# Kernel tuning notes

Measured on AMD Instinct MI355X. Metric: run time of the kernel, lower is better.

## Reference

```python
import jax, jax.numpy as jnp
import numpy as np


def setup_inputs() -> dict:
    key = jax.random.key(0)
    k1, k2, k3, k4, k5 = jax.random.split(key, 5)
    B, T_en, T_de, D, U = 8, 256, 256, 256, 256
    return {
        "en_seq": jax.random.normal(k1, (B, T_en, D), dtype=jnp.float32),
        "de_seq": jax.random.normal(k2, (B, T_de, D), dtype=jnp.float32),
        "w_en": jax.random.normal(k3, (D, U), dtype=jnp.float32) * (1.0 / np.sqrt(D)),
        "w_de": jax.random.normal(k4, (D, U), dtype=jnp.float32) * (1.0 / np.sqrt(D)),
        "nu": jax.random.normal(k5, (U, 1), dtype=jnp.float32) * (1.0 / np.sqrt(U)),
    }


def reference(en_seq, de_seq, w_en, w_de, nu):
    # Additive (Bahdanau) cross attention, faithful to the Keras layer.
    # The Keras code materializes a (B, T_de*T_en, units) tensor via
    # repeat/repeat_elements with layout index = de*T_en + en; broadcasting
    # att_en over the de axis and att_de over the en axis reproduces it.
    att_en = jnp.einsum('bed,du->beu', en_seq, w_en)       # (B, T_en, U)
    att_de = jnp.einsum('btd,du->btu', de_seq, w_de)       # (B, T_de, U)
    co_m = att_en[:, None, :, :] + att_de[:, :, None, :]   # (B, T_de, T_en, U)
    mu = jnp.einsum('bteu,uo->bteo', jnp.tanh(co_m), nu)[..., 0]  # (B, T_de, T_en)
    alphas = jax.nn.softmax(mu, axis=-1)                   # softmax over encoder steps
    sum_en = jnp.einsum('bte,bed->btd', alphas, en_seq)    # (B, T_de, D)
    return de_seq + sum_en
```

## Files before the change

kernel.cpp:

```cpp
#include <hip/hip_runtime.h>


#define C2LOG2E 2.8853900817779268f

__device__ __forceinline__ const float* uptr(const float* p) {
    unsigned long long v = (unsigned long long)p;
    unsigned lo = __builtin_amdgcn_readfirstlane((unsigned)v);
    unsigned hi = __builtin_amdgcn_readfirstlane((unsigned)(v >> 32));
    return (const float*)((((unsigned long long)hi) << 32) | lo);
}

__global__ __launch_bounds__(256, 2) void gemm2(
    const float* __restrict__ en, const float* __restrict__ de,
    const float* __restrict__ w_en, const float* __restrict__ w_de,
    float* __restrict__ att_enT, float* __restrict__ att_de)
{
    __shared__ float xs[8 * 256];

    const int isDe = blockIdx.x >> 8;
    const int rb   = blockIdx.x & 255;
    const float* x = isDe ? de : en;
    const float* w = isDe ? w_de : w_en;

    const int tid  = threadIdx.x;
    const int lane = tid & 63;
    const int wv   = __builtin_amdgcn_readfirstlane(tid >> 6);
    const int r0   = rb * 8 + wv * 2;
    const int c0   = lane << 2;

    const float* ar0 = uptr(x + r0 * 256);
    const float* ar1 = uptr(x + r0 * 256 + 256);

    float4 acc0{0,0,0,0}, acc1{0,0,0,0};

    float4 wb[4], wn[4];
    #pragma unroll
    for (int j = 0; j < 4; ++j)
        wb[j] = *(const float4*)(w + j * 256 + c0);

    for (int k0 = 0; k0 < 256; k0 += 4) {
        if (k0 < 252) {
            #pragma unroll
            for (int j = 0; j < 4; ++j)
                wn[j] = *(const float4*)(w + (k0 + 4 + j) * 256 + c0);
        }
        #pragma unroll
        for (int j = 0; j < 4; ++j) {
            const int k = k0 + j;
            const float a0 = ar0[k];
            const float a1 = ar1[k];
            acc0.x = fmaf(a0, wb[j].x, acc0.x);
            acc0.y = fmaf(a0, wb[j].y, acc0.y);
            acc0.z = fmaf(a0, wb[j].z, acc0.z);
            acc0.w = fmaf(a0, wb[j].w, acc0.w);
            acc1.x = fmaf(a1, wb[j].x, acc1.x);
            acc1.y = fmaf(a1, wb[j].y, acc1.y);
            acc1.z = fmaf(a1, wb[j].z, acc1.z);
            acc1.w = fmaf(a1, wb[j].w, acc1.w);
        }
        #pragma unroll
        for (int j = 0; j < 4; ++j) wb[j] = wn[j];
    }

    const float s = C2LOG2E;
    acc0.x *= s; acc0.y *= s; acc0.z *= s; acc0.w *= s;
    acc1.x *= s; acc1.y *= s; acc1.z *= s; acc1.w *= s;

    if (isDe) {
        float* y = att_de + r0 * 256 + c0;
        *(float4*)(y)       = acc0;
        *(float4*)(y + 256) = acc1;
    } else {
        *(float4*)&xs[(wv * 2 + 0) * 256 + c0] = acc0;
        *(float4*)&xs[(wv * 2 + 1) * 256 + c0] = acc1;
        __syncthreads();
        const int b  = rb >> 5;
        const int er = (rb & 31) * 8;
        const int u  = tid;
        float4 lo, hi;
        lo.x = xs[0 * 256 + u]; lo.y = xs[1 * 256 + u];
        lo.z = xs[2 * 256 + u]; lo.w = xs[3 * 256 + u];
        hi.x = xs[4 * 256 + u]; hi.y = xs[5 * 256 + u];
        hi.z = xs[6 * 256 + u]; hi.w = xs[7 * 256 + u];
        float* yT = att_enT + b * 65536 + u * 256 + er;
        *(float4*)(yT)     = lo;
        *(float4*)(yT + 4) = hi;
    }
}

__global__ __launch_bounds__(256, 4) void attn_kernel(
    const float* __restrict__ att_enT,
    const float* __restrict__ att_de,
    const float* __restrict__ en_seq,
    const float* __restrict__ de_seq,
    const float* __restrict__ nu,
    float* __restrict__ out)
{
    const int blk  = blockIdx.x;
    const int b    = blk & 7;
    const int t0   = (blk >> 3) << 1;
    const int tid  = threadIdx.x;
    const int lane = tid & 63;
    const int wv   = __builtin_amdgcn_readfirstlane(tid >> 6);

    __shared__ float s_mu[2][256];
    __shared__ float s_al[2][256];

    const float* aw  = att_enT + b * 65536 + (wv << 6) + lane;
    const float* ad0 = uptr(att_de + (b * 256 + t0) * 256);
    const float* ad1 = uptr(att_de + (b * 256 + t0) * 256 + 256);
    const float* nuu = uptr(nu);

    float acc0 = 0.f, acc1 = 0.f;
    float av[8], avn[8];
    #pragma unroll
    for (int j = 0; j < 8; ++j) av[j] = aw[j << 8];

    for (int u0 = 0; u0 < 256; u0 += 8) {
        if (u0 < 248) {
            #pragma unroll
            for (int j = 0; j < 8; ++j) avn[j] = aw[(u0 + 8 + j) << 8];
        }
        #pragma unroll
        for (int g = 0; g < 2; ++g) {
            const int ub = u0 + g * 4;
            const float n0 = nuu[ub + 0], n1 = nuu[ub + 1];
            const float n2 = nuu[ub + 2], n3 = nuu[ub + 3];
            const float nS01 = n0 + n1, nS23 = n2 + n3;
            const float a0 = av[g * 4 + 0], a1 = av[g * 4 + 1];
            const float a2 = av[g * 4 + 2], a3 = av[g * 4 + 3];
            {
                const float E0 = __builtin_amdgcn_exp2f(a0 + ad0[ub + 0]);
                const float E1 = __builtin_amdgcn_exp2f(a1 + ad0[ub + 1]);
                const float E2 = __builtin_amdgcn_exp2f(a2 + ad0[ub + 2]);
                const float E3 = __builtin_amdgcn_exp2f(a3 + ad0[ub + 3]);
                const float A0 = E0 + 1.f, A1 = E1 + 1.f;
                const float A2 = E2 + 1.f, A3 = E3 + 1.f;
                const float p01 = A0 * A1, p23 = A2 * A3;
                const float n01 = fmaf(n0, E1, fmaf(n1, E0, nS01));
                const float n23 = fmaf(n2, E3, fmaf(n3, E2, nS23));
                const float num = fmaf(n23, p01, n01 * p23);
                acc0 = fmaf(num, __builtin_amdgcn_rcpf(p01 * p23), acc0);
            }
            {
                const float E0 = __builtin_amdgcn_exp2f(a0 + ad1[ub + 0]);
                const float E1 = __builtin_amdgcn_exp2f(a1 + ad1[ub + 1]);
                const float E2 = __builtin_amdgcn_exp2f(a2 + ad1[ub + 2]);
                const float E3 = __builtin_amdgcn_exp2f(a3 + ad1[ub + 3]);
                const float A0 = E0 + 1.f, A1 = E1 + 1.f;
                const float A2 = E2 + 1.f, A3 = E3 + 1.f;
                const float p01 = A0 * A1, p23 = A2 * A3;
                const float n01 = fmaf(n0, E1, fmaf(n1, E0, nS01));
                const float n23 = fmaf(n2, E3, fmaf(n3, E2, nS23));
                const float num = fmaf(n23, p01, n01 * p23);
                acc1 = fmaf(num, __builtin_amdgcn_rcpf(p01 * p23), acc1);
            }
        }
        #pragma unroll
        for (int j = 0; j < 8; ++j) av[j] = avn[j];
    }
    const int eidx = (wv << 6) + lane;
    s_mu[0][eidx] = acc0;
    s_mu[1][eidx] = acc1;
    __syncthreads();

    if (wv < 2) {
        const float4 a = *(const float4*)&s_mu[wv][lane << 2];
        float mn = fminf(fminf(a.x, a.y), fminf(a.z, a.w));
        #pragma unroll
        for (int off = 32; off > 0; off >>= 1)
            mn = fminf(mn, __shfl_xor(mn, off, 64));
        const float p0 = __builtin_amdgcn_exp2f((mn - a.x) * C2LOG2E);
        const float p1 = __builtin_amdgcn_exp2f((mn - a.y) * C2LOG2E);
        const float p2 = __builtin_amdgcn_exp2f((mn - a.z) * C2LOG2E);
        const float p3 = __builtin_amdgcn_exp2f((mn - a.w) * C2LOG2E);
        float ssum = (p0 + p1) + (p2 + p3);
        #pragma unroll
        for (int off = 32; off > 0; off >>= 1)
            ssum += __shfl_xor(ssum, off, 64);
        const float inv = __builtin_amdgcn_rcpf(ssum);
        float4 al; al.x = p0 * inv; al.y = p1 * inv;
        al.z = p2 * inv; al.w = p3 * inv;
        *(float4*)&s_al[wv][lane << 2] = al;
    }
    __syncthreads();

    const float* en_b = en_seq + b * 65536 + tid;
    float o0 = 0.f, o1 = 0.f;
    for (int e0 = 0; e0 < 256; e0 += 8) {
        float v[8];
        #pragma unroll
        for (int j = 0; j < 8; ++j) v[j] = en_b[(e0 + j) << 8];
        #pragma unroll
        for (int q = 0; q < 2; ++q) {
            const int eb = e0 + q * 4;
            const float4 A0 = *(const float4*)&s_al[0][eb];
            const float4 A1 = *(const float4*)&s_al[1][eb];
            o0 = fmaf(A0.x, v[q*4+0], o0); o1 = fmaf(A1.x, v[q*4+0], o1);
            o0 = fmaf(A0.y, v[q*4+1], o0); o1 = fmaf(A1.y, v[q*4+1], o1);
            o0 = fmaf(A0.z, v[q*4+2], o0); o1 = fmaf(A1.z, v[q*4+2], o1);
            o0 = fmaf(A0.w, v[q*4+3], o0); o1 = fmaf(A1.w, v[q*4+3], o1);
        }
    }
    const int base = (b * 256 + t0) * 256 + tid;
    out[base]       = de_seq[base]       + o0;
    out[base + 256] = de_seq[base + 256] + o1;
}

extern "C" void kernel_launch(void* const* d_in, const int* in_sizes, int n_in,
                              void* d_out, int out_size, void* d_ws, size_t ws_size,
                              hipStream_t stream) {
    const float* en_seq = (const float*)d_in[0];
    const float* de_seq = (const float*)d_in[1];
    const float* w_en   = (const float*)d_in[2];
    const float* w_de   = (const float*)d_in[3];
    const float* nu     = (const float*)d_in[4];
    float* out = (float*)d_out;

    float* att_enT = (float*)d_ws;
    float* att_de  = att_enT + 8 * 256 * 256;

    gemm2<<<512, 256, 0, stream>>>(en_seq, de_seq, w_en, w_de, att_enT, att_de);
    attn_kernel<<<1024, 256, 0, stream>>>(att_enT, att_de, en_seq, de_seq,
                                          nu, out);
}
```

Measured before the change: 123.2 us.

## Precompute exponentials of projections and factor exp(a+b) into products

```diff
diff --git a/kernel.cpp b/kernel.cpp
--- a/kernel.cpp
+++ b/kernel.cpp
@@ -10,87 +10,100 @@
     return (const float*)((((unsigned long long)hi) << 32) | lo);
 }
 
-__global__ __launch_bounds__(256, 2) void gemm2(
+__global__ __launch_bounds__(256, 4) void gemm2(
     const float* __restrict__ en, const float* __restrict__ de,
     const float* __restrict__ w_en, const float* __restrict__ w_de,
-    float* __restrict__ att_enT, float* __restrict__ att_de)
+    float* __restrict__ att_enT4, float* __restrict__ att_de_exp)
 {
-    __shared__ float xs[8 * 256];
-
-    const int isDe = blockIdx.x >> 8;
-    const int rb   = blockIdx.x & 255;
+    __shared__ float part[4 * 4 * 256];
+
+    const int isDe = blockIdx.x >> 9;
+    const int rb   = blockIdx.x & 511;
     const float* x = isDe ? de : en;
     const float* w = isDe ? w_de : w_en;
 
     const int tid  = threadIdx.x;
     const int lane = tid & 63;
     const int wv   = __builtin_amdgcn_readfirstlane(tid >> 6);
-    const int r0   = rb * 8 + wv * 2;
+    const int r0   = rb * 4;
     const int c0   = lane << 2;
-
-    const float* ar0 = uptr(x + r0 * 256);
-    const float* ar1 = uptr(x + r0 * 256 + 256);
-
-    float4 acc0{0,0,0,0}, acc1{0,0,0,0};
+    const int k0   = wv << 6;
+
+    const float* ar0 = uptr(x + (r0 + 0) * 256 + k0);
+    const float* ar1 = uptr(x + (r0 + 1) * 256 + k0);
+    const float* ar2 = uptr(x + (r0 + 2) * 256 + k0);
+    const float* ar3 = uptr(x + (r0 + 3) * 256 + k0);
+    const float* wk  = w + k0 * 256 + c0;
+
+    float4 acc0{0,0,0,0}, acc1{0,0,0,0}, acc2{0,0,0,0}, acc3{0,0,0,0};
 
     float4 wb[4], wn[4];
     #pragma unroll
     for (int j = 0; j < 4; ++j)
-        wb[j] = *(const float4*)(w + j * 256 + c0);
-
-    for (int k0 = 0; k0 < 256; k0 += 4) {
-        if (k0 < 252) {
+        wb[j] = *(const float4*)(wk + j * 256);
+
+    for (int kk = 0; kk < 64; kk += 4) {
+        if (kk < 60) {
             #pragma unroll
             for (int j = 0; j < 4; ++j)
-                wn[j] = *(const float4*)(w + (k0 + 4 + j) * 256 + c0);
+                wn[j] = *(const float4*)(wk + (kk + 4 + j) * 256);
         }
         #pragma unroll
         for (int j = 0; j < 4; ++j) {
-            const int k = k0 + j;
-            const float a0 = ar0[k];
-            const float a1 = ar1[k];
-            acc0.x = fmaf(a0, wb[j].x, acc0.x);
-            acc0.y = fmaf(a0, wb[j].y, acc0.y);
-            acc0.z = fmaf(a0, wb[j].z, acc0.z);
-            acc0.w = fmaf(a0, wb[j].w, acc0.w);
-            acc1.x = fmaf(a1, wb[j].x, acc1.x);
-            acc1.y = fmaf(a1, wb[j].y, acc1.y);
-            acc1.z = fmaf(a1, wb[j].z, acc1.z);
-            acc1.w = fmaf(a1, wb[j].w, acc1.w);
+            const int k = kk + j;
+            const float a0 = ar0[k], a1 = ar1[k];
+            const float a2 = ar2[k], a3 = ar3[k];
+            acc0.x = fmaf(a0, wb[j].x, acc0.x); acc0.y = fmaf(a0, wb[j].y, acc0.y);
+            acc0.z = fmaf(a0, wb[j].z, acc0.z); acc0.w = fmaf(a0, wb[j].w, acc0.w);
+            acc1.x = fmaf(a1, wb[j].x, acc1.x); acc1.y = fmaf(a1, wb[j].y, acc1.y);
+            acc1.z = fmaf(a1, wb[j].z, acc1.z); acc1.w = fmaf(a1, wb[j].w, acc1.w);
+            acc2.x = fmaf(a2, wb[j].x, acc2.x); acc2.y = fmaf(a2, wb[j].y, acc2.y);
+            acc2.z = fmaf(a2, wb[j].z, acc2.z); acc2.w = fmaf(a2, wb[j].w, acc2.w);
+            acc3.x = fmaf(a3, wb[j].x, acc3.x); acc3.y = fmaf(a3, wb[j].y, acc3.y);
+            acc3.z = fmaf(a3, wb[j].z, acc3.z); acc3.w = fmaf(a3, wb[j].w, acc3.w);
         }
         #pragma unroll
         for (int j = 0; j < 4; ++j) wb[j] = wn[j];
     }
 
-    const float s = C2LOG2E;
-    acc0.x *= s; acc0.y *= s; acc0.z *= s; acc0.w *= s;
-    acc1.x *= s; acc1.y *= s; acc1.z *= s; acc1.w *= s;
+    *(float4*)&part[(wv * 4 + 0) * 256 + c0] = acc0;
+    *(float4*)&part[(wv * 4 + 1) * 256 + c0] = acc1;
+    *(float4*)&part[(wv * 4 + 2) * 256 + c0] = acc2;
+    *(float4*)&part[(wv * 4 + 3) * 256 + c0] = acc3;
+    __syncthreads();
+
+    const int t = tid;
+    float s[4];
+    #pragma unroll
+    for (int j = 0; j < 4; ++j) {
+        const float v = part[(0 * 4 + j) * 256 + t] + part[(1 * 4 + j) * 256 + t]
+                      + part[(2 * 4 + j) * 256 + t] + part[(3 * 4 + j) * 256 + t];
+        s[j] = __builtin_amdgcn_exp2f(v * C2LOG2E);
+    }
 
     if (isDe) {
-        float* y = att_de + r0 * 256 + c0;
-        *(float4*)(y)       = acc0;
-        *(float4*)(y + 256) = acc1;
+        const int rr0 = (rb * 4) & 2047;
+        #pragma unroll
+        for (int j = 0; j < 4; ++j)
+            att_de_exp[(rr0 + j) * 256 + t] = s[j];
     } else {
-        *(float4*)&xs[(wv * 2 + 0) * 256 + c0] = acc0;
-        *(float4*)&xs[(wv * 2 + 1) * 256 + c0] = acc1;
+        const int b  = rb >> 6;
+        const int er = (rb & 63) * 4;
         __syncthreads();
-        const int b  = rb >> 5;
-        const int er = (rb & 31) * 8;
-        const int u  = tid;
-        float4 lo, hi;
-        lo.x = xs[0 * 256 + u]; lo.y = xs[1 * 256 + u];
-        lo.z = xs[2 * 256 + u]; lo.w = xs[3 * 256 + u];
-        hi.x = xs[4 * 256 + u]; hi.y = xs[5 * 256 + u];
-        hi.z = xs[6 * 256 + u]; hi.w = xs[7 * 256 + u];
-        float* yT = att_enT + b * 65536 + u * 256 + er;
-        *(float4*)(yT)     = lo;
-        *(float4*)(yT + 4) = hi;
+        #pragma unroll
+        for (int j = 0; j < 4; ++j)
+            part[j * 256 + t] = s[j];
+        __syncthreads();
+        const int ug = t >> 2;
+        const int sl = t & 3;
+        const float4 v = *(const float4*)&part[sl * 256 + (ug << 2)];
+        *(float4*)(att_enT4 + b * 65536 + ug * 1024 + (er + sl) * 4) = v;
     }
 }
 
 __global__ __launch_bounds__(256, 4) void attn_kernel(
-    const float* __restrict__ att_enT,
-    const float* __restrict__ att_de,
+    const float* __restrict__ att_enT4,
+    const float* __restrict__ att_de_exp,
     const float* __restrict__ en_seq,
     const float* __restrict__ de_seq,
     const float* __restrict__ nu,
@@ -106,58 +119,54 @@
     __shared__ float s_mu[2][256];
     __shared__ float s_al[2][256];
 
-    const float* aw  = att_enT + b * 65536 + (wv << 6) + lane;
-    const float* ad0 = uptr(att_de + (b * 256 + t0) * 256);
-    const float* ad1 = uptr(att_de + (b * 256 + t0) * 256 + 256);
+    const float* aw  = att_enT4 + b * 65536 + (((wv << 6) + lane) << 2);
+    const float* sd0 = uptr(att_de_exp + (b * 256 + t0) * 256);
+    const float* sd1 = uptr(att_de_exp + (b * 256 + t0) * 256 + 256);
     const float* nuu = uptr(nu);
 
     float acc0 = 0.f, acc1 = 0.f;
-    float av[8], avn[8];
+    float4 cur[4], nxt[4];
     #pragma unroll
-    for (int j = 0; j < 8; ++j) av[j] = aw[j << 8];
-
-    for (int u0 = 0; u0 < 256; u0 += 8) {
-        if (u0 < 248) {
+    for (int j = 0; j < 4; ++j)
+        cur[j] = *(const float4*)(aw + j * 1024);
+
+    for (int ugb = 0; ugb < 64; ugb += 4) {
+        if (ugb < 60) {
             #pragma unroll
-            for (int j = 0; j < 8; ++j) avn[j] = aw[(u0 + 8 + j) << 8];
-        }
-        #pragma unroll
-        for (int g = 0; g < 2; ++g) {
-            const int ub = u0 + g * 4;
+            for (int j = 0; j < 4; ++j)
+                nxt[j] = *(const float4*)(aw + (ugb + 4 + j) * 1024);
+        }
+        #pragma unroll
+        for (int j = 0; j < 4; ++j) {
+            const int ub = (ugb + j) << 2;
             const float n0 = nuu[ub + 0], n1 = nuu[ub + 1];
             const float n2 = nuu[ub + 2], n3 = nuu[ub + 3];
-            const float nS01 = n0 + n1, nS23 = n2 + n3;
-            const float a0 = av[g * 4 + 0], a1 = av[g * 4 + 1];
-            const float a2 = av[g * 4 + 2], a3 = av[g * 4 + 3];
+            const float4 Ea = cur[j];
             {
-                const float E0 = __builtin_amdgcn_exp2f(a0 + ad0[ub + 0]);
-                const float E1 = __builtin_amdgcn_exp2f(a1 + ad0[ub + 1]);
-                const float E2 = __builtin_amdgcn_exp2f(a2 + ad0[ub + 2]);
-                const float E3 = __builtin_amdgcn_exp2f(a3 + ad0[ub + 3]);
-                const float A0 = E0 + 1.f, A1 = E1 + 1.f;
-                const float A2 = E2 + 1.f, A3 = E3 + 1.f;
+                const float A0 = fmaf(Ea.x, sd0[ub + 0], 1.f);
+                const float A1 = fmaf(Ea.y, sd0[ub + 1], 1.f);
+                const float A2 = fmaf(Ea.z, sd0[ub + 2], 1.f);
+                const float A3 = fmaf(Ea.w, sd0[ub + 3], 1.f);
                 const float p01 = A0 * A1, p23 = A2 * A3;
-                const float n01 = fmaf(n0, E1, fmaf(n1, E0, nS01));
-                const float n23 = fmaf(n2, E3, fmaf(n3, E2, nS23));
-                const float num = fmaf(n23, p01, n01 * p23);
+                const float n01 = fmaf(n0, A1, n1 * A0);
+                const float n23 = fmaf(n2, A3, n3 * A2);
+                const float num = fmaf(n01, p23, n23 * p01);
                 acc0 = fmaf(num, __builtin_amdgcn_rcpf(p01 * p23), acc0);
             }
             {
-                const float E0 = __builtin_amdgcn_exp2f(a0 + ad1[ub + 0]);
-                const float E1 = __builtin_amdgcn_exp2f(a1 + ad1[ub + 1]);
-                const float E2 = __builtin_amdgcn_exp2f(a2 + ad1[ub + 2]);
-                const float E3 = __builtin_amdgcn_exp2f(a3 + ad1[ub + 3]);
-                const float A0 = E0 + 1.f, A1 = E1 + 1.f;
-                const float A2 = E2 + 1.f, A3 = E3 + 1.f;
+                const float A0 = fmaf(Ea.x, sd1[ub + 0], 1.f);
+                const float A1 = fmaf(Ea.y, sd1[ub + 1], 1.f);
+                const float A2 = fmaf(Ea.z, sd1[ub + 2], 1.f);
+                const float A3 = fmaf(Ea.w, sd1[ub + 3], 1.f);
                 const float p01 = A0 * A1, p23 = A2 * A3;
-                const float n01 = fmaf(n0, E1, fmaf(n1, E0, nS01));
-                const float n23 = fmaf(n2, E3, fmaf(n3, E2, nS23));
-                const float num = fmaf(n23, p01, n01 * p23);
+                const float n01 = fmaf(n0, A1, n1 * A0);
+                const float n23 = fmaf(n2, A3, n3 * A2);
+                const float num = fmaf(n01, p23, n23 * p01);
                 acc1 = fmaf(num, __builtin_amdgcn_rcpf(p01 * p23), acc1);
             }
         }
         #pragma unroll
-        for (int j = 0; j < 8; ++j) av[j] = avn[j];
+        for (int j = 0; j < 4; ++j) cur[j] = nxt[j];
     }
     const int eidx = (wv << 6) + lane;
     s_mu[0][eidx] = acc0;
@@ -217,10 +226,11 @@
     const float* nu     = (const float*)d_in[4];
     float* out = (float*)d_out;
 
-    float* att_enT = (float*)d_ws;
-    float* att_de  = att_enT + 8 * 256 * 256;
-
-    gemm2<<<512, 256, 0, stream>>>(en_seq, de_seq, w_en, w_de, att_enT, att_de);
-    attn_kernel<<<1024, 256, 0, stream>>>(att_enT, att_de, en_seq, de_seq,
-                                          nu, out);
-}
+    float* att_enT4   = (float*)d_ws;
+    float* att_de_exp = att_enT4 + 8 * 256 * 256;
+
+    gemm2<<<1024, 256, 0, stream>>>(en_seq, de_seq, w_en, w_de,
+                                    att_enT4, att_de_exp);
+    attn_kernel<<<1024, 256, 0, stream>>>(att_enT4, att_de_exp, en_seq,
+                                          de_seq, nu, out);
+}
```

Measured after the change: 112.3 us, median of 2. 8.8% less time.
